# Kernel tuning notes

Measured on AMD Instinct MI355X. Metric: run time of the kernel, lower is better.

Reference implementation:

```python
import jax, jax.numpy as jnp
import numpy as np

L = 1024
D = 512      # d_model
H = 256      # hidden


def setup_inputs() -> dict:
    key = jax.random.key(0)
    k1, k2, k3, k4, k5 = jax.random.split(key, 5)
    scale = 0.02
    return {
        "seq_feats": jax.random.normal(k1, (L, D), dtype=jnp.float32),
        "W1": jax.random.normal(k2, (H, 2 * D), dtype=jnp.float32) * scale,
        "b1": jax.random.normal(k3, (H,), dtype=jnp.float32) * scale,
        "W2": jax.random.normal(k4, (1, H), dtype=jnp.float32) * scale,
        "b2": jax.random.normal(k5, (1,), dtype=jnp.float32) * scale,
    }


def reference(seq_feats, W1, b1, W2, b2):
    # cat([a, b]) @ W1.T == a @ W1[:, :D].T + b @ W1[:, D:].T
    # so we never materialize the [L, L, 2D] concat tensor.
    d = seq_feats.shape[1]
    pa = seq_feats @ W1[:, :d].T          # [L, H] (row / i contribution)
    pb = seq_feats @ W1[:, d:].T          # [L, H] (col / j contribution)
    h = jax.nn.relu(pa[:, None, :] + pb[None, :, :] + b1)  # [L, L, H]
    scores = jnp.einsum("ijh,h->ij", h, W2[0]) + b2[0]      # [L, L]
    scores = (scores + scores.T) * 0.5
    return jax.nn.sigmoid(scores)
```

## Files before the change

kernel.cpp:

```cpp
#include <hip/hip_runtime.h>
#include <hip/hip_bf16.h>
#include <math.h>

#define LL 1024
#define DD 512
#define HH 256


__device__ __forceinline__ ushort f2bf(float f) {
  __hip_bfloat16 h = __float2bfloat16(f);
  return *reinterpret_cast<ushort*>(&h);
}
__device__ __forceinline__ float bfu(ushort u) {
  return __uint_as_float(((unsigned int)u) << 16);
}

__global__ __launch_bounds__(512) void sp_gemm(
    const float* __restrict__ S, const float* __restrict__ W1,
    float* __restrict__ pC) {
  __shared__ float Sl[2][128][36];
  __shared__ float Wl[2][64][36];

  const int tid = threadIdx.x;
  const int tx  = tid & 15;
  const int ty  = tid >> 4;
  const int i0  = blockIdx.x * 128;
  const int n0  = blockIdx.y * 64;
  const int kz  = blockIdx.z * 128;

  const int srow = tid >> 3;
  const int ssl  = tid & 7;
  const int wn   = n0 + srow;
  const float* s0 = S + (size_t)(i0 + srow) * DD + kz + 4 * ssl;
  const float* s1 = S + (size_t)(i0 + 64 + srow) * DD + kz + 4 * ssl;
  const float* w0 = W1 + (size_t)(wn & 255) * (2 * DD) + (wn >> 8) * DD + kz + 4 * ssl;

  float4 sA, sB, wA;
  auto ld = [&](int c) {
    sA = *(const float4*)(s0 + 32 * c);
    sB = *(const float4*)(s1 + 32 * c);
    wA = *(const float4*)(w0 + 32 * c);
  };
  auto st = [&](int b) {
    *(float4*)&Sl[b][srow][4 * ssl]      = sA;
    *(float4*)&Sl[b][64 + srow][4 * ssl] = sB;
    *(float4*)&Wl[b][srow][4 * ssl]      = wA;
  };

  float acc[4][4] = {{0.f}};

  ld(0); st(0); __syncthreads();

  for (int c = 0; c < 4; ++c) {
    const int cur = c & 1;
    if (c < 3) ld(c + 1);
    #pragma unroll 2
    for (int k4 = 0; k4 < 8; ++k4) {
      float4 wf[4], sf[4];
      #pragma unroll
      for (int b = 0; b < 4; ++b) wf[b] = *(const float4*)&Wl[cur][tx + 16 * b][4 * k4];
      #pragma unroll
      for (int a = 0; a < 4; ++a) sf[a] = *(const float4*)&Sl[cur][4 * ty + a][4 * k4];
      #pragma unroll
      for (int a = 0; a < 4; ++a) {
        #pragma unroll
        for (int b = 0; b < 4; ++b) {
          acc[a][b] += sf[a].x * wf[b].x + sf[a].y * wf[b].y +
                       sf[a].z * wf[b].z + sf[a].w * wf[b].w;
        }
      }
    }
    if (c < 3) st(cur ^ 1);
    __syncthreads();
  }

  float* base = pC + (size_t)blockIdx.z * (512 * LL);
  #pragma unroll
  for (int b = 0; b < 4; ++b) {
    const int n = n0 + tx + 16 * b;
    *(float4*)(base + (size_t)n * LL + i0 + 4 * ty) =
        make_float4(acc[0][b], acc[1][b], acc[2][b], acc[3][b]);
  }
}

__global__ __launch_bounds__(256) void sp_reduce(
    const float* __restrict__ pC, const float* __restrict__ b1,
    ushort* __restrict__ O) {
  const int m = blockIdx.x * 256 + threadIdx.x;
  const int n = m >> 8;
  const int NW = 512 * 256;
  const float4* p = (const float4*)pC + m;
  float4 a  = p[0];
  const float4 v1 = p[NW], v2 = p[2 * NW], v3 = p[3 * NW];
  a.x += v1.x + v2.x + v3.x;
  a.y += v1.y + v2.y + v3.y;
  a.z += v1.z + v2.z + v3.z;
  a.w += v1.w + v2.w + v3.w;
  if (n < 256) {
    const float bb = b1[n];
    a.x += bb; a.y += bb; a.z += bb; a.w += bb;
  }
  ushort4 o;
  o.x = f2bf(a.x); o.y = f2bf(a.y); o.z = f2bf(a.z); o.w = f2bf(a.w);
  *(ushort4*)(O + 4 * (size_t)m) = o;
}

__global__ __launch_bounds__(512) void sp_pairwise(
    const ushort* __restrict__ O, const float* __restrict__ W2,
    float* __restrict__ pz) {
  __shared__ float Tl[128][72];
  __shared__ float Ul[128][72];
  __shared__ float PR[4][128];
  __shared__ float As[64], Bs[64];

  const int tid = threadIdx.x;
  const int tx  = tid & 15;
  const int ty  = tid >> 4;
  const int j0  = blockIdx.x * 64;
  const int i0  = blockIdx.y * 64;
  const int hz  = blockIdx.z * 128;

  #pragma unroll
  for (int q = 0; q < 4; ++q) {
    const int m = q * 512 + tid;
    const int hh = m >> 4;
    const int g4 = (m & 15) * 4;
    const ushort4 tv = *(const ushort4*)(O + (size_t)(hz + hh) * LL + i0 + g4);
    const ushort4 uv = *(const ushort4*)(O + (size_t)(HH + hz + hh) * LL + j0 + g4);
    *(float4*)&Tl[hh][g4] = make_float4(bfu(tv.x), bfu(tv.y), bfu(tv.z), bfu(tv.w));
    *(float4*)&Ul[hh][g4] = make_float4(bfu(uv.x), bfu(uv.y), bfu(uv.z), bfu(uv.w));
  }
  __syncthreads();

  {
    const int x = tid & 127, hs = tid >> 7;
    const float* pan = (x < 64) ? &Tl[0][x] : &Ul[0][x - 64];
    float p = 0.f;
    #pragma unroll 8
    for (int n = 0; n < 32; ++n) {
      const int hh = hs * 32 + n;
      p = fmaf(pan[hh * 72], W2[hz + hh], p);
    }
    PR[hs][x] = p;
  }
  __syncthreads();
  if (tid < 128) {
    const float s = PR[0][tid] + PR[1][tid] + PR[2][tid] + PR[3][tid];
    if (tid < 64) As[tid] = s; else Bs[tid - 64] = s;
  }
  __syncthreads();

  float a0[4] = {0.f, 0.f, 0.f, 0.f};
  float a1[4] = {0.f, 0.f, 0.f, 0.f};

  #pragma unroll 4
  for (int hh = 0; hh < 128; ++hh) {
    const float2 tv = *(const float2*)&Tl[hh][2 * ty];
    const float4 uv = *(const float4*)&Ul[hh][4 * tx];
    const float w = W2[hz + hh];
    a0[0] = fmaf(fabsf(tv.x + uv.x), w, a0[0]);
    a0[1] = fmaf(fabsf(tv.x + uv.y), w, a0[1]);
    a0[2] = fmaf(fabsf(tv.x + uv.z), w, a0[2]);
    a0[3] = fmaf(fabsf(tv.x + uv.w), w, a0[3]);
    a1[0] = fmaf(fabsf(tv.y + uv.x), w, a1[0]);
    a1[1] = fmaf(fabsf(tv.y + uv.y), w, a1[1]);
    a1[2] = fmaf(fabsf(tv.y + uv.z), w, a1[2]);
    a1[3] = fmaf(fabsf(tv.y + uv.w), w, a1[3]);
  }

  const float A0 = As[2 * ty], A1 = As[2 * ty + 1];
  const float B0 = Bs[4 * tx], B1 = Bs[4 * tx + 1];
  const float B2 = Bs[4 * tx + 2], B3 = Bs[4 * tx + 3];
  float* po = pz + (size_t)blockIdx.z * ((size_t)LL * LL)
                 + (size_t)(i0 + 2 * ty) * LL + j0 + 4 * tx;
  *(float4*)po = make_float4(a0[0] + A0 + B0, a0[1] + A0 + B1,
                             a0[2] + A0 + B2, a0[3] + A0 + B3);
  *(float4*)(po + LL) = make_float4(a1[0] + A1 + B0, a1[1] + A1 + B1,
                                    a1[2] + A1 + B2, a1[3] + A1 + B3);
}

__global__ __launch_bounds__(1024) void sp_symsig(
    const float* __restrict__ pz, const float* __restrict__ b2,
    float* __restrict__ out) {
  __shared__ float B[64][65];
  const int i0 = blockIdx.y * 64;
  const int j0 = blockIdx.x * 64;
  const int r  = threadIdx.x >> 4;
  const int g  = threadIdx.x & 15;
  const size_t L2 = (size_t)LL * LL;

  const float* pm = pz + (size_t)(j0 + r) * LL + i0 + 4 * g;
  const float4 m0 = *(const float4*)(pm);
  const float4 m1 = *(const float4*)(pm + L2);
  B[r][4 * g + 0] = m0.x + m1.x;
  B[r][4 * g + 1] = m0.y + m1.y;
  B[r][4 * g + 2] = m0.z + m1.z;
  B[r][4 * g + 3] = m0.w + m1.w;
  __syncthreads();

  const float* pd = pz + (size_t)(i0 + r) * LL + j0 + 4 * g;
  const float4 d0 = *(const float4*)(pd);
  const float4 d1 = *(const float4*)(pd + L2);
  const float bb = b2[0];
  float4 o;
  float x;
  x = 0.25f * (d0.x + d1.x + B[4 * g + 0][r]) + bb; o.x = 1.f / (1.f + expf(-x));
  x = 0.25f * (d0.y + d1.y + B[4 * g + 1][r]) + bb; o.y = 1.f / (1.f + expf(-x));
  x = 0.25f * (d0.z + d1.z + B[4 * g + 2][r]) + bb; o.z = 1.f / (1.f + expf(-x));
  x = 0.25f * (d0.w + d1.w + B[4 * g + 3][r]) + bb; o.w = 1.f / (1.f + expf(-x));
  *(float4*)(out + (size_t)(i0 + r) * LL + j0 + 4 * g) = o;
}

extern "C" void kernel_launch(void* const* d_in, const int* in_sizes, int n_in,
                              void* d_out, int out_size, void* d_ws, size_t ws_size,
                              hipStream_t stream) {
  const float* S  = (const float*)d_in[0];
  const float* W1 = (const float*)d_in[1];
  const float* b1 = (const float*)d_in[2];
  const float* W2 = (const float*)d_in[3];
  const float* b2 = (const float*)d_in[4];
  float* out = (float*)d_out;

  float* ws = (float*)d_ws;
  float* pC = ws;
  ushort* O = (ushort*)(ws + 4 * 512 * LL);
  float* pz = ws + 4 * 512 * LL + 262144;

  hipLaunchKernelGGL(sp_gemm, dim3(8, 8, 4), dim3(512), 0, stream,
                     S, W1, pC);
  hipLaunchKernelGGL(sp_reduce, dim3(512), dim3(256), 0, stream,
                     pC, b1, O);
  hipLaunchKernelGGL(sp_pairwise, dim3(16, 16, 2), dim3(512), 0, stream,
                     O, W2, pz);
  hipLaunchKernelGGL(sp_symsig, dim3(16, 16), dim3(1024), 0, stream,
                     pz, b2, out);
}
```

Measured before the change: 46.08 us.

## Replace split-K FP32 GEMM and reduce with bf16 MFMA GEMM plus conversion pass

Drops the split-K fp32 SIMT GEMM and its separate reduction kernel. A new pass converts S and W1 to bf16, and a GEMM built on the MFMA 16x16x32 bf16 intrinsic computes the projection in one go, adding b1 in its epilogue. This removes the partial-sum buffer round trip and uses matrix cores. In exchange, the inputs are rounded to bf16 before the GEMM, which lowers precision. The MFMA kernel also reads straight from global memory without LDS staging and writes scattered 2-byte stores.

```diff
diff --git a/kernel.cpp b/kernel.cpp
--- a/kernel.cpp
+++ b/kernel.cpp
@@ -6,6 +6,9 @@
 #define DD 512
 #define HH 256
 
+typedef __attribute__((ext_vector_type(8))) short bf16x8;
+typedef __attribute__((ext_vector_type(4))) float f32x4;
+
 
 __device__ __forceinline__ ushort f2bf(float f) {
   __hip_bfloat16 h = __float2bfloat16(f);
@@ -15,94 +18,58 @@
   return __uint_as_float(((unsigned int)u) << 16);
 }
 
-__global__ __launch_bounds__(512) void sp_gemm(
+__global__ __launch_bounds__(256) void sp_convert(
     const float* __restrict__ S, const float* __restrict__ W1,
-    float* __restrict__ pC) {
-  __shared__ float Sl[2][128][36];
-  __shared__ float Wl[2][64][36];
-
-  const int tid = threadIdx.x;
-  const int tx  = tid & 15;
-  const int ty  = tid >> 4;
-  const int i0  = blockIdx.x * 128;
-  const int n0  = blockIdx.y * 64;
-  const int kz  = blockIdx.z * 128;
-
-  const int srow = tid >> 3;
-  const int ssl  = tid & 7;
-  const int wn   = n0 + srow;
-  const float* s0 = S + (size_t)(i0 + srow) * DD + kz + 4 * ssl;
-  const float* s1 = S + (size_t)(i0 + 64 + srow) * DD + kz + 4 * ssl;
-  const float* w0 = W1 + (size_t)(wn & 255) * (2 * DD) + (wn >> 8) * DD + kz + 4 * ssl;
-
-  float4 sA, sB, wA;
-  auto ld = [&](int c) {
-    sA = *(const float4*)(s0 + 32 * c);
-    sB = *(const float4*)(s1 + 32 * c);
-    wA = *(const float4*)(w0 + 32 * c);
-  };
-  auto st = [&](int b) {
-    *(float4*)&Sl[b][srow][4 * ssl]      = sA;
-    *(float4*)&Sl[b][64 + srow][4 * ssl] = sB;
-    *(float4*)&Wl[b][srow][4 * ssl]      = wA;
-  };
-
-  float acc[4][4] = {{0.f}};
-
-  ld(0); st(0); __syncthreads();
-
-  for (int c = 0; c < 4; ++c) {
-    const int cur = c & 1;
-    if (c < 3) ld(c + 1);
-    #pragma unroll 2
-    for (int k4 = 0; k4 < 8; ++k4) {
-      float4 wf[4], sf[4];
-      #pragma unroll
-      for (int b = 0; b < 4; ++b) wf[b] = *(const float4*)&Wl[cur][tx + 16 * b][4 * k4];
-      #pragma unroll
-      for (int a = 0; a < 4; ++a) sf[a] = *(const float4*)&Sl[cur][4 * ty + a][4 * k4];
-      #pragma unroll
-      for (int a = 0; a < 4; ++a) {
-        #pragma unroll
-        for (int b = 0; b < 4; ++b) {
-          acc[a][b] += sf[a].x * wf[b].x + sf[a].y * wf[b].y +
-                       sf[a].z * wf[b].z + sf[a].w * wf[b].w;
-        }
-      }
-    }
-    if (c < 3) st(cur ^ 1);
-    __syncthreads();
-  }
-
-  float* base = pC + (size_t)blockIdx.z * (512 * LL);
+    ushort* __restrict__ Sb, ushort* __restrict__ Wb) {
+  const int m = blockIdx.x * 256 + threadIdx.x;
+  const int NS = (LL * DD) / 4;
+  if (m < NS) {
+    const float4 v = ((const float4*)S)[m];
+    ushort4 o;
+    o.x = f2bf(v.x); o.y = f2bf(v.y); o.z = f2bf(v.z); o.w = f2bf(v.w);
+    ((ushort4*)Sb)[m] = o;
+  } else {
+    const int w  = m - NS;
+    const int n  = w >> 7;
+    const int kg = w & 127;
+    const float4 v = *(const float4*)(W1 + (size_t)(n & 255) * 1024 +
+                                      (n >> 8) * 512 + 4 * kg);
+    ushort4 o;
+    o.x = f2bf(v.x); o.y = f2bf(v.y); o.z = f2bf(v.z); o.w = f2bf(v.w);
+    *(ushort4*)(Wb + (size_t)n * 512 + 4 * kg) = o;
+  }
+}
+
+__global__ __launch_bounds__(256) void sp_mgemm(
+    const ushort* __restrict__ Wb, const ushort* __restrict__ Sb,
+    const float* __restrict__ b1, ushort* __restrict__ O) {
+  const int tid  = threadIdx.x;
+  const int lane = tid & 63;
+  const int wv   = tid >> 6;
+  const int i0   = blockIdx.x * 32 + (wv >> 1) * 16;
+  const int n0   = blockIdx.y * 32 + (wv & 1) * 16;
+  const int lr   = lane & 15;
+  const int lg   = lane >> 4;
+
+  const ushort* ap = Wb + (size_t)(n0 + lr) * 512 + lg * 8;
+  const ushort* bp = Sb + (size_t)(i0 + lr) * 512 + lg * 8;
+
+  f32x4 acc = {0.f, 0.f, 0.f, 0.f};
   #pragma unroll
-  for (int b = 0; b < 4; ++b) {
-    const int n = n0 + tx + 16 * b;
-    *(float4*)(base + (size_t)n * LL + i0 + 4 * ty) =
-        make_float4(acc[0][b], acc[1][b], acc[2][b], acc[3][b]);
-  }
-}
-
-__global__ __launch_bounds__(256) void sp_reduce(
-    const float* __restrict__ pC, const float* __restrict__ b1,
-    ushort* __restrict__ O) {
-  const int m = blockIdx.x * 256 + threadIdx.x;
-  const int n = m >> 8;
-  const int NW = 512 * 256;
-  const float4* p = (const float4*)pC + m;
-  float4 a  = p[0];
-  const float4 v1 = p[NW], v2 = p[2 * NW], v3 = p[3 * NW];
-  a.x += v1.x + v2.x + v3.x;
-  a.y += v1.y + v2.y + v3.y;
-  a.z += v1.z + v2.z + v3.z;
-  a.w += v1.w + v2.w + v3.w;
-  if (n < 256) {
-    const float bb = b1[n];
-    a.x += bb; a.y += bb; a.z += bb; a.w += bb;
-  }
-  ushort4 o;
-  o.x = f2bf(a.x); o.y = f2bf(a.y); o.z = f2bf(a.z); o.w = f2bf(a.w);
-  *(ushort4*)(O + 4 * (size_t)m) = o;
+  for (int ks = 0; ks < 512; ks += 32) {
+    const bf16x8 af = *(const bf16x8*)(ap + ks);
+    const bf16x8 bf = *(const bf16x8*)(bp + ks);
+    acc = __builtin_amdgcn_mfma_f32_16x16x32_bf16(af, bf, acc, 0, 0, 0);
+  }
+
+  const bool hasB = (n0 < 256);
+  #pragma unroll
+  for (int r = 0; r < 4; ++r) {
+    const int n = n0 + lg * 4 + r;
+    float v = acc[r];
+    if (hasB) v += b1[n];
+    O[(size_t)n * LL + i0 + lr] = f2bf(v);
+  }
 }
 
 __global__ __launch_bounds__(512) void sp_pairwise(
@@ -222,14 +189,15 @@
   float* out = (float*)d_out;
 
   float* ws = (float*)d_ws;
-  float* pC = ws;
-  ushort* O = (ushort*)(ws + 4 * 512 * LL);
-  float* pz = ws + 4 * 512 * LL + 262144;
-
-  hipLaunchKernelGGL(sp_gemm, dim3(8, 8, 4), dim3(512), 0, stream,
-                     S, W1, pC);
-  hipLaunchKernelGGL(sp_reduce, dim3(512), dim3(256), 0, stream,
-                     pC, b1, O);
+  ushort* Sb = (ushort*)ws;
+  ushort* Wb = (ushort*)(ws + 262144);
+  ushort* O  = (ushort*)(ws + 393216);
+  float*  pz = ws + 655360;
+
+  hipLaunchKernelGGL(sp_convert, dim3(768), dim3(256), 0, stream,
+                     S, W1, Sb, Wb);
+  hipLaunchKernelGGL(sp_mgemm, dim3(32, 16), dim3(256), 0, stream,
+                     Wb, Sb, b1, O);
   hipLaunchKernelGGL(sp_pairwise, dim3(16, 16, 2), dim3(512), 0, stream,
                      O, W2, pz);
   hipLaunchKernelGGL(sp_symsig, dim3(16, 16), dim3(1024), 0, stream,
```

New measurement: 46.39 us. Within noise of the previous version (+0.7%).
